# Kernel tuning notes

Hardware: AMD Instinct MI355X
Metric: run time of the kernel (lower is better)

Reference implementation:

```python
import jax, jax.numpy as jnp
import numpy as np

B, T, D_IN, D_OUT = 4, 2048, 1024, 1024

def setup_inputs() -> dict:
    key = jax.random.key(0)
    k0, k1, k2, k3 = jax.random.split(key, 4)
    s = 1.0 / np.sqrt(D_IN)
    return {
        "x": jax.random.normal(k0, (B, T, D_IN), dtype=jnp.float32),
        "w_query": jax.random.normal(k1, (D_OUT, D_IN), dtype=jnp.float32) * s,
        "w_key": jax.random.normal(k2, (D_OUT, D_IN), dtype=jnp.float32) * s,
        "w_value": jax.random.normal(k3, (D_OUT, D_IN), dtype=jnp.float32) * s,
    }

def reference(x, w_query, w_key, w_value):
    # Linear (no bias): y = x @ W.T, W has shape (d_out, d_in)
    q = jnp.einsum('btd,od->bto', x, w_query)   # (B,T,d_out)
    k = jnp.einsum('btd,od->bto', x, w_key)
    v = jnp.einsum('btd,od->bto', x, w_value)
    scale = 1.0 / jnp.sqrt(jnp.asarray(k.shape[-1], dtype=x.dtype))
    scores = jnp.einsum('bqo,bko->bqk', q, k) * scale  # (B,T,T)
    t = scores.shape[-1]
    causal = jnp.tril(jnp.ones((t, t), dtype=bool))    # True = keep
    scores = jnp.where(causal, scores, -jnp.inf)
    weights = jax.nn.softmax(scores, axis=-1)
    # dropout rate is 0.0 -> identity
    context = jnp.einsum('bqk,bko->bqo', weights, v)   # (B,T,d_out)
    return context
```

## Files before the change

kernel.cpp:

```cpp
#include <hip/hip_runtime.h>
#include <hip/hip_bf16.h>

#define NB 4
#define TT 2048
#define DD 1024
#define MM (NB*TT)

using f32x4  = __attribute__((ext_vector_type(4))) float;
using bf16x8 = __attribute__((ext_vector_type(8))) __bf16;
using u16x8  = __attribute__((ext_vector_type(8))) unsigned short;

__device__ __forceinline__ unsigned short f2b(float f) {
  __hip_bfloat16 h = __float2bfloat16(f);
  return *reinterpret_cast<unsigned short*>(&h);
}

__device__ __forceinline__ float b2f(unsigned short u) {
  __hip_bfloat16 h = *reinterpret_cast<__hip_bfloat16*>(&u);
  return __bfloat162float(h);
}

__device__ __forceinline__ void gld_lds16(const void* g, void* l) {
  __builtin_amdgcn_global_load_lds(
      (const __attribute__((address_space(1))) void*)g,
      (__attribute__((address_space(3))) void*)l, 16, 0, 0);
}

__global__ void k_cvt4(const float* __restrict__ x,  const float* __restrict__ wq,
                       const float* __restrict__ wk, const float* __restrict__ wv,
                       unsigned short* __restrict__ xb, unsigned short* __restrict__ wqb,
                       unsigned short* __restrict__ wkb, unsigned short* __restrict__ wvb) {
  const int nx = MM*DD/4, nw = DD*DD/4;
  const int ntot = nx + 3*nw;
  int i = blockIdx.x * blockDim.x + threadIdx.x;
  int stride = gridDim.x * blockDim.x;
  for (; i < ntot; i += stride) {
    const float* s; unsigned short* d; int j;
    if (i < nx)            { s = x;  d = xb;  j = i; }
    else if (i < nx + nw)  { s = wq; d = wqb; j = i - nx; }
    else if (i < nx + 2*nw){ s = wk; d = wkb; j = i - nx - nw; }
    else                   { s = wv; d = wvb; j = i - nx - 2*nw; }
    float4 v = reinterpret_cast<const float4*>(s)[j];
    ushort4 o;
    o.x = f2b(v.x); o.y = f2b(v.y); o.z = f2b(v.z); o.w = f2b(v.w);
    reinterpret_cast<ushort4*>(d)[j] = o;
  }
}

__launch_bounds__(256)
__global__ void k_qkv(const unsigned short* __restrict__ xb,
                      const unsigned short* __restrict__ wqb,
                      const unsigned short* __restrict__ wkb,
                      const unsigned short* __restrict__ wvb,
                      unsigned short* __restrict__ Qb,
                      unsigned short* __restrict__ Kb,
                      unsigned short* __restrict__ Vt) {
  __shared__ __align__(16) unsigned short As[128*64];
  __shared__ __align__(16) unsigned short Bs[128*64];
  const int tid = threadIdx.x;
  const int l = tid & 63, wid = tid >> 6;
  const int z = blockIdx.z;
  const unsigned short* W = (z == 0) ? wqb : (z == 1) ? wkb : wvb;
  unsigned short* out = (z == 0) ? Qb : (z == 1) ? Kb : Vt;
  const long m0 = (long)blockIdx.x * 128;
  const long n0 = (long)blockIdx.y * 128;
  const int l15 = l & 15, l4 = l >> 4;
  const int wr = (wid >> 1) * 64, wc = (wid & 1) * 64;

  const int srow = wid * 8 + (l >> 3);
  const int scol = 8 * ((l & 7) ^ (l >> 3));
  const unsigned short* Ap = xb + (m0 + srow) * DD + scol;
  const unsigned short* Wp = W  + (n0 + srow) * DD + scol;
  unsigned short* AsW = &As[wid * 512];
  unsigned short* BsW = &Bs[wid * 512];

  f32x4 acc[4][4] = {};

  for (int k0 = 0; k0 < DD; k0 += 64) {
    __syncthreads();
    #pragma unroll
    for (int u = 0; u < 4; ++u) {
      gld_lds16(Ap + (size_t)u*32*DD + k0, AsW + u*2048);
      gld_lds16(Wp + (size_t)u*32*DD + k0, BsW + u*2048);
    }
    __syncthreads();
    #pragma unroll
    for (int kk = 0; kk < 2; ++kk) {
      bf16x8 af[4], bfr[4];
      #pragma unroll
      for (int mi = 0; mi < 4; ++mi) {
        int ro = wr + mi*16 + l15;
        int off = ro*128 + ((kk*64 + l4*16) ^ ((ro & 7) << 4));
        af[mi] = *reinterpret_cast<const bf16x8*>((const char*)As + off);
      }
      #pragma unroll
      for (int ni = 0; ni < 4; ++ni) {
        int ro = wc + ni*16 + l15;
        int off = ro*128 + ((kk*64 + l4*16) ^ ((ro & 7) << 4));
        bfr[ni] = *reinterpret_cast<const bf16x8*>((const char*)Bs + off);
      }
      #pragma unroll
      for (int mi = 0; mi < 4; ++mi)
        #pragma unroll
        for (int ni = 0; ni < 4; ++ni)
          acc[mi][ni] = __builtin_amdgcn_mfma_f32_16x16x32_bf16(af[mi], bfr[ni], acc[mi][ni], 0, 0, 0);
    }
  }

  if (z < 2) {
    #pragma unroll
    for (int mi = 0; mi < 4; ++mi)
      #pragma unroll
      for (int ni = 0; ni < 4; ++ni)
        #pragma unroll
        for (int r = 0; r < 4; ++r) {
          long row = m0 + wr + mi*16 + l4*4 + r;
          long col = n0 + wc + ni*16 + l15;
          out[row * DD + col] = f2b(acc[mi][ni][r]);
        }
  } else {
    #pragma unroll
    for (int mi = 0; mi < 4; ++mi)
      #pragma unroll
      for (int ni = 0; ni < 4; ++ni)
        #pragma unroll
        for (int r = 0; r < 4; ++r) {
          long row = m0 + wr + mi*16 + l4*4 + r;
          long col = n0 + wc + ni*16 + l15;
          long b = row >> 11, t = row & (TT - 1);
          out[(b * DD + col) * TT + t] = f2b(acc[mi][ni][r]);
        }
  }
}

__launch_bounds__(256)
__global__ void k_scores(const unsigned short* __restrict__ Qb,
                         const unsigned short* __restrict__ Kb,
                         unsigned short* __restrict__ S) {
  __shared__ __align__(16) unsigned short As[128*32];
  __shared__ __align__(16) unsigned short Bs[128*32];
  const int tid = threadIdx.x;
  const int l = tid & 63, wid = tid >> 6;
  const int l15 = l & 15, l4 = l >> 4;
  const int wr = (wid >> 1) * 64, wc = (wid & 1) * 64;

  const int bid = blockIdx.x;
  const int swz = (bid & 7) * 68 + (bid >> 3);
  const int b = swz / 136;
  int t = swz % 136;
  int qi = 0;
  while ((qi + 1) * (qi + 2) / 2 <= t) qi++;
  const int ki = t - qi * (qi + 1) / 2;

  const size_t arow0 = (size_t)b * TT + qi * 128;
  const size_t brow0 = (size_t)b * TT + ki * 128;

  const int lrow = tid >> 2;
  const int lcol = (tid & 3) * 8;
  const unsigned short* Ap = Qb + (arow0 + lrow) * DD + lcol;
  const unsigned short* Bp = Kb + (brow0 + lrow) * DD + lcol;
  unsigned short* AsW = &As[wid * 512];
  unsigned short* BsW = &Bs[wid * 512];

  f32x4 acc[4][4] = {};

  for (int k0 = 0; k0 < DD; k0 += 32) {
    __syncthreads();
    gld_lds16(Ap + k0,           AsW);
    gld_lds16(Ap + 64*DD + k0,   AsW + 2048);
    gld_lds16(Bp + k0,           BsW);
    gld_lds16(Bp + 64*DD + k0,   BsW + 2048);
    __syncthreads();
    bf16x8 af[4], bfr[4];
    #pragma unroll
    for (int mi = 0; mi < 4; ++mi)
      af[mi] = *reinterpret_cast<const bf16x8*>(&As[(wr + mi*16 + l15)*32 + l4*8]);
    #pragma unroll
    for (int ni = 0; ni < 4; ++ni)
      bfr[ni] = *reinterpret_cast<const bf16x8*>(&Bs[(wc + ni*16 + l15)*32 + l4*8]);
    #pragma unroll
    for (int mi = 0; mi < 4; ++mi)
      #pragma unroll
      for (int ni = 0; ni < 4; ++ni)
        acc[mi][ni] = __builtin_amdgcn_mfma_f32_16x16x32_bf16(af[mi], bfr[ni], acc[mi][ni], 0, 0, 0);
  }

  const float scale = 0.03125f;
  #pragma unroll
  for (int mi = 0; mi < 4; ++mi)
    #pragma unroll
    for (int ni = 0; ni < 4; ++ni)
      #pragma unroll
      for (int r = 0; r < 4; ++r) {
        int row = wr + mi*16 + l4*4 + r;
        int col = wc + ni*16 + l15;
        int gq = qi*128 + row, gk = ki*128 + col;
        float v = (gk > gq) ? -1e30f : acc[mi][ni][r] * scale;
        S[((size_t)b * TT + gq) * TT + gk] = f2b(v);
      }
}

__launch_bounds__(256)
__global__ void k_softmax(unsigned short* __restrict__ S, float* __restrict__ rl) {
  const int tid = threadIdx.x;
  const int w = tid >> 6, l = tid & 63;
  const int row = blockIdx.x * 4 + w;
  const int b = row >> 11, q = row & (TT - 1);
  unsigned short* Srow = S + ((size_t)b * TT + q) * TT;
  const int width = ((q >> 7) + 1) << 7;

  float v[4][8];
  bool has[4];
  float mx = -1e30f;
  #pragma unroll
  for (int c = 0; c < 4; ++c) {
    const int off = c * 512 + l * 8;
    has[c] = off < width;
    if (has[c]) {
      u16x8 u = *reinterpret_cast<const u16x8*>(&Srow[off]);
      #pragma unroll
      for (int j = 0; j < 8; ++j) { v[c][j] = b2f(u[j]); mx = fmaxf(mx, v[c][j]); }
    }
  }
  #pragma unroll
  for (int mm = 1; mm < 64; mm <<= 1) mx = fmaxf(mx, __shfl_xor(mx, mm));

  float s = 0.f;
  #pragma unroll
  for (int c = 0; c < 4; ++c) {
    if (has[c]) {
      u16x8 u;
      #pragma unroll
      for (int j = 0; j < 8; ++j) {
        float p = __expf(v[c][j] - mx);
        s += p;
        u[j] = f2b(p);
      }
      *reinterpret_cast<u16x8*>(&Srow[c * 512 + l * 8]) = u;
    }
  }
  #pragma unroll
  for (int mm = 1; mm < 64; mm <<= 1) s += __shfl_xor(s, mm);
  if (l == 0) rl[row] = 1.0f / s;
}

__launch_bounds__(256)
__global__ void k_pv(const unsigned short* __restrict__ P,
                     const unsigned short* __restrict__ Vt,
                     const float* __restrict__ rl,
                     float* __restrict__ O) {
  __shared__ __align__(16) unsigned short As[128*32];
  __shared__ __align__(16) unsigned short Bs[128*32];
  const int tid = threadIdx.x;
  const int l = tid & 63, wid = tid >> 6;
  const int l15 = l & 15, l4 = l >> 4;
  const int wr = (wid >> 1) * 64, wc = (wid & 1) * 64;

  const int qi = 15 - (blockIdx.x >> 5);
  const int di = (blockIdx.x >> 2) & 7;
  const int b  = blockIdx.x & 3;
  const int KEXT = (qi + 1) * 128;

  const int lrow = tid >> 2;
  const int lcol = (tid & 3) * 8;
  const unsigned short* Ap = P  + ((size_t)b * TT + qi * 128 + lrow) * TT + lcol;
  const unsigned short* Bp = Vt + ((size_t)b * DD + di * 128 + lrow) * TT + lcol;
  unsigned short* AsW = &As[wid * 512];
  unsigned short* BsW = &Bs[wid * 512];

  f32x4 acc[4][4] = {};

  for (int k0 = 0; k0 < KEXT; k0 += 32) {
    __syncthreads();
    gld_lds16(Ap + k0,           AsW);
    gld_lds16(Ap + 64*TT + k0,   AsW + 2048);
    gld_lds16(Bp + k0,           BsW);
    gld_lds16(Bp + 64*TT + k0,   BsW + 2048);
    __syncthreads();
    bf16x8 af[4], bfr[4];
    #pragma unroll
    for (int mi = 0; mi < 4; ++mi)
      af[mi] = *reinterpret_cast<const bf16x8*>(&As[(wr + mi*16 + l15)*32 + l4*8]);
    #pragma unroll
    for (int ni = 0; ni < 4; ++ni)
      bfr[ni] = *reinterpret_cast<const bf16x8*>(&Bs[(wc + ni*16 + l15)*32 + l4*8]);
    #pragma unroll
    for (int mi = 0; mi < 4; ++mi)
      #pragma unroll
      for (int ni = 0; ni < 4; ++ni)
        acc[mi][ni] = __builtin_amdgcn_mfma_f32_16x16x32_bf16(af[mi], bfr[ni], acc[mi][ni], 0, 0, 0);
  }

  #pragma unroll
  for (int mi = 0; mi < 4; ++mi)
    #pragma unroll
    for (int ni = 0; ni < 4; ++ni)
      #pragma unroll
      for (int r = 0; r < 4; ++r) {
        int row = wr + mi*16 + l4*4 + r;
        int col = wc + ni*16 + l15;
        size_t q = (size_t)qi * 128 + row;
        O[((size_t)b * TT + q) * DD + di * 128 + col] =
            acc[mi][ni][r] * rl[(size_t)b * TT + q];
      }
}

extern "C" void kernel_launch(void* const* d_in, const int* in_sizes, int n_in,
                              void* d_out, int out_size, void* d_ws, size_t ws_size,
                              hipStream_t stream) {
  const float* x  = (const float*)d_in[0];
  const float* wq = (const float*)d_in[1];
  const float* wk = (const float*)d_in[2];
  const float* wv = (const float*)d_in[3];
  unsigned short* ws  = (unsigned short*)d_ws;
  unsigned short* Qb  = ws;
  unsigned short* Kb  = Qb + (size_t)MM * DD;
  unsigned short* Vt  = Kb + (size_t)MM * DD;
  unsigned short* Sb  = Vt + (size_t)MM * DD;
  unsigned short* xb  = Sb;
  unsigned short* wqb = xb + (size_t)MM * DD;
  unsigned short* wkb = wqb + (size_t)DD * DD;
  unsigned short* wvb = wkb + (size_t)DD * DD;
  float* rl = (float*)(Sb + (size_t)NB * TT * TT);
  float* out = (float*)d_out;

  k_cvt4<<<2048, 256, 0, stream>>>(x, wq, wk, wv, xb, wqb, wkb, wvb);
  k_qkv<<<dim3(MM/128, DD/128, 3), 256, 0, stream>>>(xb, wqb, wkb, wvb, Qb, Kb, Vt);
  k_scores<<<544, 256, 0, stream>>>(Qb, Kb, Sb);
  k_softmax<<<MM/4, 256, 0, stream>>>(Sb, rl);
  k_pv<<<512, 256, 0, stream>>>(Sb, Vt, rl, out);
}
```

Baseline: 160.3 us.

## Double K-tile depth and XOR-swizzle LDS layout in scores and PV GEMMs

Raises the K step of the scores and PV GEMM main loops from 32 to 64, which halves the number of barrier pairs per output tile. The LDS tile now uses 128-byte rows with an XOR swizzle: global-to-LDS loads pre-permute the column chunk, and the fragment reads apply the matching XOR to avoid LDS bank conflicts. LDS use per block doubles, which may reduce occupancy. The swizzle indexing must match exactly between writes and reads to stay correct.

```diff
diff --git a/kernel.cpp b/kernel.cpp
--- a/kernel.cpp
+++ b/kernel.cpp
@@ -137,8 +137,8 @@
 __global__ void k_scores(const unsigned short* __restrict__ Qb,
                          const unsigned short* __restrict__ Kb,
                          unsigned short* __restrict__ S) {
-  __shared__ __align__(16) unsigned short As[128*32];
-  __shared__ __align__(16) unsigned short Bs[128*32];
+  __shared__ __align__(16) unsigned short As[128*64];
+  __shared__ __align__(16) unsigned short Bs[128*64];
   const int tid = threadIdx.x;
   const int l = tid & 63, wid = tid >> 6;
   const int l15 = l & 15, l4 = l >> 4;
@@ -155,34 +155,44 @@
   const size_t arow0 = (size_t)b * TT + qi * 128;
   const size_t brow0 = (size_t)b * TT + ki * 128;
 
-  const int lrow = tid >> 2;
-  const int lcol = (tid & 3) * 8;
-  const unsigned short* Ap = Qb + (arow0 + lrow) * DD + lcol;
-  const unsigned short* Bp = Kb + (brow0 + lrow) * DD + lcol;
+  const int srow = wid * 8 + (l >> 3);
+  const int scol = 8 * ((l & 7) ^ (l >> 3));
+  const unsigned short* Ap = Qb + (arow0 + srow) * DD + scol;
+  const unsigned short* Bp = Kb + (brow0 + srow) * DD + scol;
   unsigned short* AsW = &As[wid * 512];
   unsigned short* BsW = &Bs[wid * 512];
 
   f32x4 acc[4][4] = {};
 
-  for (int k0 = 0; k0 < DD; k0 += 32) {
-    __syncthreads();
-    gld_lds16(Ap + k0,           AsW);
-    gld_lds16(Ap + 64*DD + k0,   AsW + 2048);
-    gld_lds16(Bp + k0,           BsW);
-    gld_lds16(Bp + 64*DD + k0,   BsW + 2048);
-    __syncthreads();
-    bf16x8 af[4], bfr[4];
-    #pragma unroll
-    for (int mi = 0; mi < 4; ++mi)
-      af[mi] = *reinterpret_cast<const bf16x8*>(&As[(wr + mi*16 + l15)*32 + l4*8]);
-    #pragma unroll
-    for (int ni = 0; ni < 4; ++ni)
-      bfr[ni] = *reinterpret_cast<const bf16x8*>(&Bs[(wc + ni*16 + l15)*32 + l4*8]);
-    #pragma unroll
-    for (int mi = 0; mi < 4; ++mi)
-      #pragma unroll
-      for (int ni = 0; ni < 4; ++ni)
-        acc[mi][ni] = __builtin_amdgcn_mfma_f32_16x16x32_bf16(af[mi], bfr[ni], acc[mi][ni], 0, 0, 0);
+  for (int k0 = 0; k0 < DD; k0 += 64) {
+    __syncthreads();
+    #pragma unroll
+    for (int u = 0; u < 4; ++u) {
+      gld_lds16(Ap + (size_t)u*32*DD + k0, AsW + u*2048);
+      gld_lds16(Bp + (size_t)u*32*DD + k0, BsW + u*2048);
+    }
+    __syncthreads();
+    #pragma unroll
+    for (int kk = 0; kk < 2; ++kk) {
+      bf16x8 af[4], bfr[4];
+      #pragma unroll
+      for (int mi = 0; mi < 4; ++mi) {
+        int ro = wr + mi*16 + l15;
+        int off = ro*128 + ((kk*64 + l4*16) ^ ((ro & 7) << 4));
+        af[mi] = *reinterpret_cast<const bf16x8*>((const char*)As + off);
+      }
+      #pragma unroll
+      for (int ni = 0; ni < 4; ++ni) {
+        int ro = wc + ni*16 + l15;
+        int off = ro*128 + ((kk*64 + l4*16) ^ ((ro & 7) << 4));
+        bfr[ni] = *reinterpret_cast<const bf16x8*>((const char*)Bs + off);
+      }
+      #pragma unroll
+      for (int mi = 0; mi < 4; ++mi)
+        #pragma unroll
+        for (int ni = 0; ni < 4; ++ni)
+          acc[mi][ni] = __builtin_amdgcn_mfma_f32_16x16x32_bf16(af[mi], bfr[ni], acc[mi][ni], 0, 0, 0);
+    }
   }
 
   const float scale = 0.03125f;
@@ -249,8 +259,8 @@
                      const unsigned short* __restrict__ Vt,
                      const float* __restrict__ rl,
                      float* __restrict__ O) {
-  __shared__ __align__(16) unsigned short As[128*32];
-  __shared__ __align__(16) unsigned short Bs[128*32];
+  __shared__ __align__(16) unsigned short As[128*64];
+  __shared__ __align__(16) unsigned short Bs[128*64];
   const int tid = threadIdx.x;
   const int l = tid & 63, wid = tid >> 6;
   const int l15 = l & 15, l4 = l >> 4;
@@ -261,34 +271,44 @@
   const int b  = blockIdx.x & 3;
   const int KEXT = (qi + 1) * 128;
 
-  const int lrow = tid >> 2;
-  const int lcol = (tid & 3) * 8;
-  const unsigned short* Ap = P  + ((size_t)b * TT + qi * 128 + lrow) * TT + lcol;
-  const unsigned short* Bp = Vt + ((size_t)b * DD + di * 128 + lrow) * TT + lcol;
+  const int srow = wid * 8 + (l >> 3);
+  const int scol = 8 * ((l & 7) ^ (l >> 3));
+  const unsigned short* Ap = P  + ((size_t)b * TT + qi * 128 + srow) * TT + scol;
+  const unsigned short* Bp = Vt + ((size_t)b * DD + di * 128 + srow) * TT + scol;
   unsigned short* AsW = &As[wid * 512];
   unsigned short* BsW = &Bs[wid * 512];
 
   f32x4 acc[4][4] = {};
 
-  for (int k0 = 0; k0 < KEXT; k0 += 32) {
-    __syncthreads();
-    gld_lds16(Ap + k0,           AsW);
-    gld_lds16(Ap + 64*TT + k0,   AsW + 2048);
-    gld_lds16(Bp + k0,           BsW);
-    gld_lds16(Bp + 64*TT + k0,   BsW + 2048);
-    __syncthreads();
-    bf16x8 af[4], bfr[4];
-    #pragma unroll
-    for (int mi = 0; mi < 4; ++mi)
-      af[mi] = *reinterpret_cast<const bf16x8*>(&As[(wr + mi*16 + l15)*32 + l4*8]);
-    #pragma unroll
-    for (int ni = 0; ni < 4; ++ni)
-      bfr[ni] = *reinterpret_cast<const bf16x8*>(&Bs[(wc + ni*16 + l15)*32 + l4*8]);
-    #pragma unroll
-    for (int mi = 0; mi < 4; ++mi)
-      #pragma unroll
-      for (int ni = 0; ni < 4; ++ni)
-        acc[mi][ni] = __builtin_amdgcn_mfma_f32_16x16x32_bf16(af[mi], bfr[ni], acc[mi][ni], 0, 0, 0);
+  for (int k0 = 0; k0 < KEXT; k0 += 64) {
+    __syncthreads();
+    #pragma unroll
+    for (int u = 0; u < 4; ++u) {
+      gld_lds16(Ap + (size_t)u*32*TT + k0, AsW + u*2048);
+      gld_lds16(Bp + (size_t)u*32*TT + k0, BsW + u*2048);
+    }
+    __syncthreads();
+    #pragma unroll
+    for (int kk = 0; kk < 2; ++kk) {
+      bf16x8 af[4], bfr[4];
+      #pragma unroll
+      for (int mi = 0; mi < 4; ++mi) {
+        int ro = wr + mi*16 + l15;
+        int off = ro*128 + ((kk*64 + l4*16) ^ ((ro & 7) << 4));
+        af[mi] = *reinterpret_cast<const bf16x8*>((const char*)As + off);
+      }
+      #pragma unroll
+      for (int ni = 0; ni < 4; ++ni) {
+        int ro = wc + ni*16 + l15;
+        int off = ro*128 + ((kk*64 + l4*16) ^ ((ro & 7) << 4));
+        bfr[ni] = *reinterpret_cast<const bf16x8*>((const char*)Bs + off);
+      }
+      #pragma unroll
+      for (int mi = 0; mi < 4; ++mi)
+        #pragma unroll
+        for (int ni = 0; ni < 4; ++ni)
+          acc[mi][ni] = __builtin_amdgcn_mfma_f32_16x16x32_bf16(af[mi], bfr[ni], acc[mi][ni], 0, 0, 0);
+    }
   }
 
   #pragma unroll
```

After: 158.6 us. No clear change (-1.0%).
